# Kernel optimization log

Measured on AMD Instinct MI355X. Metric: run time of the kernel, lower is better.

## Reference

```python
import jax, jax.numpy as jnp
import numpy as np

B, N, DIM, HEADS = 1, 4096, 1024, 16
HEAD_DIM = DIM // HEADS
SCALE = HEAD_DIM ** -0.5
GRID = 64  # GRID*GRID == N, power-of-2 Hilbert grid


def _hilbert_d2xy(n, d):
    # standard Hilbert curve distance->(x,y), vectorized in numpy
    rx = np.zeros_like(d)
    ry = np.zeros_like(d)
    x = np.zeros_like(d)
    y = np.zeros_like(d)
    t = d.copy()
    s = 1
    while s < n:
        rx = (t // 2) & 1
        ry = (t ^ rx) & 1
        # rotate
        swap = ry == 0
        flip = swap & (rx == 1)
        x_f = np.where(flip, s - 1 - x, x)
        y_f = np.where(flip, s - 1 - y, y)
        x, y = np.where(swap, y_f, x_f), np.where(swap, x_f, y_f)
        x = x + s * rx
        y = y + s * ry
        t = t // 4
        s *= 2
    return x, y


def _hilbert_indices(n_tokens, grid):
    d = np.arange(n_tokens)
    hx, hy = _hilbert_d2xy(grid, d)
    # token at Hilbert distance d lives at row-major position hy*grid+hx
    return (hy * grid + hx).astype(np.int32)


def setup_inputs() -> dict:
    key = jax.random.key(0)
    k1, k2, k3 = jax.random.split(key, 3)
    x = jax.random.normal(k1, (B, N, DIM), dtype=jnp.float32)
    w_qkv = jax.random.normal(k2, (3 * DIM, DIM), dtype=jnp.float32) * (DIM ** -0.5)
    w_out = jax.random.normal(k3, (DIM, DIM), dtype=jnp.float32) * (DIM ** -0.5)
    indices = jnp.asarray(_hilbert_indices(N, GRID))
    return {"x": x, "w_qkv": w_qkv, "w_out": w_out, "indices": indices}


def reference(x, w_qkv, w_out, indices):
    b, n, c = x.shape
    # qkv projection: nn.Linear -> x @ W^T, reshape to [B,N,3,H,Dh]
    qkv = jnp.einsum("bnc,dc->bnd", x, w_qkv).reshape(b, n, 3, HEADS, HEAD_DIM)
    q, k, v = qkv[:, :, 0], qkv[:, :, 1], qkv[:, :, 2]  # each [B,N,H,Dh]
    # Hilbert gather along sequence
    q = q[:, indices]
    k = k[:, indices]
    v = v[:, indices]
    # full softmax attention per head
    scores = jnp.einsum("bnhd,bmhd->bhnm", q, k) * SCALE
    attn = jax.nn.softmax(scores, axis=-1)
    out = jnp.einsum("bhnm,bmhd->bnhd", attn, v)  # [B,N,H,Dh]
    # scatter back to original order
    inv = jnp.argsort(indices)
    out = out[:, inv].reshape(b, n, c)
    return jnp.einsum("bnc,dc->bnd", out, w_out)
```

## Files before the change

kernel.cpp:

```cpp
#include <hip/hip_runtime.h>
#include <stdint.h>

#define NTOK 4096
#define HD 64
#define DIMC 1024

typedef __attribute__((ext_vector_type(8))) short s16x8;
typedef __attribute__((ext_vector_type(4))) float f32x4;

#if __has_builtin(__builtin_amdgcn_exp2f)
#define EXP2(x) __builtin_amdgcn_exp2f(x)
#else
#define EXP2(x) exp2f(x)
#endif

__device__ inline unsigned short f2bf(float f) {
  union { float f; unsigned u; } v; v.f = f;
  unsigned r = v.u + 0x7FFFu + ((v.u >> 16) & 1u);
  return (unsigned short)(r >> 16);
}

__device__ inline unsigned cvt_pk_bf16(float lo, float hi) {
  unsigned r;
  asm("v_cvt_pk_bf16_f32 %0, %1, %2" : "=v"(r) : "v"(lo), "v"(hi));
  return r;
}

__device__ inline float bf2f(unsigned short u) {
  union { unsigned u; float f; } v; v.u = ((unsigned)u) << 16;
  return v.f;
}

__device__ inline void gld16(const void* g, void* s) {
  __builtin_amdgcn_global_load_lds((const __attribute__((address_space(1))) void*)g,
                                   (__attribute__((address_space(3))) void*)s, 16, 0, 0);
}

#define N4_X   1048576
#define N4_WQ  786432
#define N4_WO  262144
__global__ void cvt_all(const float4* __restrict__ x, const float4* __restrict__ wq,
                        const float4* __restrict__ wo, ushort4* __restrict__ xb,
                        ushort4* __restrict__ wqb, ushort4* __restrict__ wob) {
  int i = blockIdx.x * 256 + threadIdx.x;
  const float4* s; ushort4* d; int off;
  if (i < N4_X) { s = x; d = xb; off = i; }
  else if (i < N4_X + N4_WQ) { s = wq; d = wqb; off = i - N4_X; }
  else { s = wo; d = wob; off = i - (N4_X + N4_WQ); }
  float4 v = s[off];
  ushort4 o;
  o.x = f2bf(v.x); o.y = f2bf(v.y); o.z = f2bf(v.z); o.w = f2bf(v.w);
  d[off] = o;
}

#define QSCALE 0.18033688011112042f
__global__ __launch_bounds__(256) void gemm_qkv(
    const unsigned short* __restrict__ A,
    const unsigned short* __restrict__ B,
    unsigned short* __restrict__ qb,
    unsigned short* __restrict__ kb,
    unsigned short* __restrict__ vtb)
{
  __shared__ unsigned short As[128 * 32];
  __shared__ unsigned short Bs[128 * 32];
  const int t = threadIdx.x;
  const int l = t & 63;
  const int w = t >> 6;
  const int wr = w >> 1, wc = w & 1;
  const int bm = blockIdx.x, bn = blockIdx.y;
  const int K = 1024;

  f32x4 acc[4][4];
#pragma unroll
  for (int m = 0; m < 4; ++m)
#pragma unroll
    for (int n = 0; n < 4; ++n)
#pragma unroll
      for (int r = 0; r < 4; ++r) acc[m][n][r] = 0.f;

  for (int kt = 0; kt < K; kt += 32) {
    __syncthreads();
#pragma unroll
    for (int j = 0; j < 2; ++j) {
      const int o = j * 4096 + t * 16;
      const int row = o >> 6;
      const int cole = (o & 63) >> 1;
      gld16(A + (size_t)(bm * 128 + row) * K + kt + cole, (char*)As + o);
      gld16(B + (size_t)(bn * 128 + row) * K + kt + cole, (char*)Bs + o);
    }
    __syncthreads();
    s16x8 af[4], bfr[4];
    const int cb = (l >> 4) * 16;
#pragma unroll
    for (int m = 0; m < 4; ++m)
      af[m] = *(const s16x8*)((const char*)As + (wr * 64 + m * 16 + (l & 15)) * 64 + cb);
#pragma unroll
    for (int n = 0; n < 4; ++n)
      bfr[n] = *(const s16x8*)((const char*)Bs + (wc * 64 + n * 16 + (l & 15)) * 64 + cb);
#pragma unroll
    for (int m = 0; m < 4; ++m)
#pragma unroll
      for (int n = 0; n < 4; ++n)
        acc[m][n] = __builtin_amdgcn_mfma_f32_16x16x32_bf16(af[m], bfr[n], acc[m][n], 0, 0, 0);
  }

#pragma unroll
  for (int m = 0; m < 4; ++m) {
#pragma unroll
    for (int n = 0; n < 4; ++n) {
#pragma unroll
      for (int r = 0; r < 4; ++r) {
        const int gm = bm * 128 + wr * 64 + m * 16 + (l >> 4) * 4 + r;
        const int gn = bn * 128 + wc * 64 + n * 16 + (l & 15);
        const float val = acc[m][n][r];
        const int part = gn >> 10;
        const int h = (gn >> 6) & 15;
        const int dd = gn & 63;
        if (part == 0)      qb[((size_t)h * NTOK + gm) * HD + dd] = f2bf(val * QSCALE);
        else if (part == 1) kb[((size_t)h * NTOK + gm) * HD + dd] = f2bf(val);
        else                vtb[((size_t)h * HD + dd) * NTOK + gm] = f2bf(val);
      }
    }
  }
}

__global__ __launch_bounds__(128, 4) void fa_split(
    const unsigned short* __restrict__ Q,
    const unsigned short* __restrict__ Kin,
    const unsigned short* __restrict__ Vt,
    unsigned short* __restrict__ Opart,
    float* __restrict__ Lpart)
{
  __shared__ unsigned short Ks[2][32 * 64];
  __shared__ unsigned short Vs[2][64 * 32];

  const int t = threadIdx.x, l = t & 63, w = t >> 6;
  const int g = l >> 4, q = l & 15;
  const int wg = blockIdx.x;
  const int h = wg & 15;
  const int qt = (wg >> 4) & 63;
  const int half = wg >> 10;
  const int q0 = qt * 64 + w * 32;
  const int kbase0 = half * (NTOK / 2);
  const unsigned short* Qh = Q + (size_t)h * NTOK * HD;
  const unsigned short* Kh = Kin + (size_t)h * NTOK * HD;
  const unsigned short* Vh = Vt + (size_t)h * HD * NTOK;

  int offK[2], offV[2];
#pragma unroll
  for (int j = 0; j < 2; ++j) {
    const int o = j * 2048 + t * 16;
    const int rho = o >> 7;
    const int c = o & 127;
    const int n = ((rho & 12) << 1) | ((rho & 16) >> 2) | (rho & 3);
    offK[j] = n * 128 + (c ^ ((rho & 7) << 4));
    const int rv = o >> 6;
    const int cv = o & 63;
    offV[j] = rv * (NTOK * 2) + (cv ^ (((rv >> 1) & 3) << 4));
  }

  s16x8 qf[2][2];
#pragma unroll
  for (int rb = 0; rb < 2; ++rb)
#pragma unroll
    for (int tq = 0; tq < 2; ++tq)
      qf[rb][tq] = *(const s16x8*)(Qh + (size_t)(q0 + rb * 16 + q) * HD + tq * 32 + g * 8);

  s16x8 ones;
#pragma unroll
  for (int i = 0; i < 8; ++i) ones[i] = (short)0x3F80;

  f32x4 oacc[2][4], lacc[2];
#pragma unroll
  for (int rb = 0; rb < 2; ++rb) {
#pragma unroll
    for (int db = 0; db < 4; ++db)
#pragma unroll
      for (int r = 0; r < 4; ++r) oacc[rb][db][r] = 0.f;
#pragma unroll
    for (int r = 0; r < 4; ++r) lacc[rb][r] = 0.f;
  }

#pragma unroll
  for (int j = 0; j < 2; ++j) {
    const int o = j * 2048 + t * 16;
    gld16((const char*)Kh + (size_t)kbase0 * 128 + offK[j], (char*)Ks[0] + o);
    gld16((const char*)Vh + (size_t)kbase0 * 2 + offV[j], (char*)Vs[0] + o);
  }
  __syncthreads();

  int cur = 0;
  const int NIT = (NTOK / 2) / 32;
  for (int it = 0; it < NIT; ++it) {
    if (it + 1 < NIT) {
      const char* kp = (const char*)Kh + (size_t)(kbase0 + (it + 1) * 32) * 128;
      const char* vp = (const char*)Vh + (size_t)(kbase0 + (it + 1) * 32) * 2;
#pragma unroll
      for (int j = 0; j < 2; ++j) {
        const int o = j * 2048 + t * 16;
        gld16(kp + offK[j], (char*)Ks[cur ^ 1] + o);
        gld16(vp + offV[j], (char*)Vs[cur ^ 1] + o);
      }
    }

    const char* kb = (const char*)Ks[cur];
    const char* vb = (const char*)Vs[cur];

    f32x4 sc[2][2];
    __builtin_amdgcn_s_setprio(1);
#pragma unroll
    for (int kb2 = 0; kb2 < 2; ++kb2) {
      const int row = kb2 * 16 + q;
      const int swz = (row & 7) << 4;
      s16x8 kf0 = *(const s16x8*)(kb + row * 128 + ((g * 16) ^ swz));
      s16x8 kf1 = *(const s16x8*)(kb + row * 128 + ((64 + g * 16) ^ swz));
#pragma unroll
      for (int rb = 0; rb < 2; ++rb) {
        f32x4 z = {0.f, 0.f, 0.f, 0.f};
        z = __builtin_amdgcn_mfma_f32_16x16x32_bf16(kf0, qf[rb][0], z, 0, 0, 0);
        sc[rb][kb2] = __builtin_amdgcn_mfma_f32_16x16x32_bf16(kf1, qf[rb][1], z, 0, 0, 0);
      }
    }
    __builtin_amdgcn_s_setprio(0);

    union PU { unsigned u[4]; s16x8 v; } pu[2];
#pragma unroll
    for (int rb = 0; rb < 2; ++rb) {
      pu[rb].u[0] = cvt_pk_bf16(EXP2(sc[rb][0][0]), EXP2(sc[rb][0][1]));
      pu[rb].u[1] = cvt_pk_bf16(EXP2(sc[rb][0][2]), EXP2(sc[rb][0][3]));
      pu[rb].u[2] = cvt_pk_bf16(EXP2(sc[rb][1][0]), EXP2(sc[rb][1][1]));
      pu[rb].u[3] = cvt_pk_bf16(EXP2(sc[rb][1][2]), EXP2(sc[rb][1][3]));
    }

    __builtin_amdgcn_s_setprio(1);
    const int vswz = ((q >> 1) & 3) << 4;
#pragma unroll
    for (int db = 0; db < 4; ++db) {
      const int row = db * 16 + q;
      s16x8 vf = *(const s16x8*)(vb + row * 64 + ((g * 16) ^ vswz));
#pragma unroll
      for (int rb = 0; rb < 2; ++rb)
        oacc[rb][db] = __builtin_amdgcn_mfma_f32_16x16x32_bf16(vf, pu[rb].v, oacc[rb][db], 0, 0, 0);
    }
#pragma unroll
    for (int rb = 0; rb < 2; ++rb)
      lacc[rb] = __builtin_amdgcn_mfma_f32_16x16x32_bf16(ones, pu[rb].v, lacc[rb], 0, 0, 0);
    __builtin_amdgcn_s_setprio(0);

    __syncthreads();
    cur ^= 1;
  }

  const size_t pbase = ((size_t)(half * 16 + h) * NTOK);
#pragma unroll
  for (int rb = 0; rb < 2; ++rb) {
    const int nn = q0 + rb * 16 + q;
#pragma unroll
    for (int db = 0; db < 4; ++db) {
      uint2 pr;
      pr.x = cvt_pk_bf16(oacc[rb][db][0], oacc[rb][db][1]);
      pr.y = cvt_pk_bf16(oacc[rb][db][2], oacc[rb][db][3]);
      *(uint2*)(Opart + (pbase + nn) * HD + db * 16 + g * 4) = pr;
    }
    if (g == 0) Lpart[pbase + nn] = lacc[rb][0];
  }
}

__global__ __launch_bounds__(256) void gemm_out(
    const unsigned short* __restrict__ Opart,
    const float* __restrict__ Lpart,
    const unsigned short* __restrict__ Bw,
    float* __restrict__ outf)
{
  __shared__ unsigned short As[128 * 32];
  __shared__ unsigned short Bs[128 * 32];
  const int t = threadIdx.x;
  const int l = t & 63;
  const int w = t >> 6;
  const int wr = w >> 1, wc = w & 1;
  const int bm = blockIdx.x, bn = blockIdx.y;

  f32x4 acc[4][4];
#pragma unroll
  for (int m = 0; m < 4; ++m)
#pragma unroll
    for (int n = 0; n < 4; ++n)
#pragma unroll
      for (int r = 0; r < 4; ++r) acc[m][n][r] = 0.f;

  for (int kt = 0; kt < 1024; kt += 32) {
    __syncthreads();
#pragma unroll
    for (int j = 0; j < 2; ++j) {
      const int o = j * 4096 + t * 16;
      const int row = o >> 6;
      const int cole = (o & 63) >> 1;
      gld16(Bw + (size_t)(bn * 128 + row) * 1024 + kt + cole, (char*)Bs + o);
      const int kg = kt + cole;
      const int hh = kg >> 6, dd = kg & 63;
      const int mm = bm * 128 + row;
      const size_t base = ((size_t)hh * NTOK + mm) * HD + dd;
      s16x8 p0 = *(const s16x8*)(Opart + base);
      s16x8 p1 = *(const s16x8*)(Opart + base + (size_t)16 * NTOK * HD);
      const float inv = 1.f / (Lpart[(size_t)hh * NTOK + mm] +
                               Lpart[(size_t)16 * NTOK + (size_t)hh * NTOK + mm]);
      union PA { unsigned u[4]; s16x8 v; } pa;
#pragma unroll
      for (int e = 0; e < 4; ++e)
        pa.u[e] = cvt_pk_bf16((bf2f((unsigned short)p0[2 * e]) + bf2f((unsigned short)p1[2 * e])) * inv,
                              (bf2f((unsigned short)p0[2 * e + 1]) + bf2f((unsigned short)p1[2 * e + 1])) * inv);
      *(s16x8*)((char*)As + o) = pa.v;
    }
    __syncthreads();
    s16x8 af[4], bfr[4];
    const int cb = (l >> 4) * 16;
#pragma unroll
    for (int m = 0; m < 4; ++m)
      af[m] = *(const s16x8*)((const char*)As + (wr * 64 + m * 16 + (l & 15)) * 64 + cb);
#pragma unroll
    for (int n = 0; n < 4; ++n)
      bfr[n] = *(const s16x8*)((const char*)Bs + (wc * 64 + n * 16 + (l & 15)) * 64 + cb);
#pragma unroll
    for (int m = 0; m < 4; ++m)
#pragma unroll
      for (int n = 0; n < 4; ++n)
        acc[m][n] = __builtin_amdgcn_mfma_f32_16x16x32_bf16(af[m], bfr[n], acc[m][n], 0, 0, 0);
  }

#pragma unroll
  for (int m = 0; m < 4; ++m)
#pragma unroll
    for (int n = 0; n < 4; ++n)
#pragma unroll
      for (int r = 0; r < 4; ++r) {
        const int gm = bm * 128 + wr * 64 + m * 16 + (l >> 4) * 4 + r;
        const int gn = bn * 128 + wc * 64 + n * 16 + (l & 15);
        outf[(size_t)gm * 1024 + gn] = acc[m][n][r];
      }
}

extern "C" void kernel_launch(void* const* d_in, const int* in_sizes, int n_in,
                              void* d_out, int out_size, void* d_ws, size_t ws_size,
                              hipStream_t stream) {
  const float* x    = (const float*)d_in[0];
  const float* wqkv = (const float*)d_in[1];
  const float* wout = (const float*)d_in[2];
  float* out = (float*)d_out;
  char* ws = (char*)d_ws;

  unsigned short* Opart = (unsigned short*)(ws);
  unsigned short* xb    = (unsigned short*)(ws);
  unsigned short* wqkvb = (unsigned short*)(ws + 8388608);
  float*          Lp    = (float*)(ws + 16777216);
  unsigned short* Qb    = (unsigned short*)(ws + 17825792);
  unsigned short* Kb    = (unsigned short*)(ws + 26214400);
  unsigned short* Vtb   = (unsigned short*)(ws + 34603008);
  unsigned short* woutb = (unsigned short*)(ws + 42991616);

  cvt_all<<<8192, 256, 0, stream>>>((const float4*)x, (const float4*)wqkv, (const float4*)wout,
                                    (ushort4*)xb, (ushort4*)wqkvb, (ushort4*)woutb);

  gemm_qkv<<<dim3(32, 24), 256, 0, stream>>>(xb, wqkvb, Qb, Kb, Vtb);

  fa_split<<<2048, 128, 0, stream>>>(Qb, Kb, Vtb, Opart, Lp);

  gemm_out<<<dim3(32, 8), 256, 0, stream>>>(Opart, Lp, woutb, out);
}
```

Measured before the change: 170.3 us.

## Enlarge attention query tile, split keys four ways, add separate combine kernel

```diff
diff --git a/kernel.cpp b/kernel.cpp
--- a/kernel.cpp
+++ b/kernel.cpp
@@ -38,15 +38,12 @@
 
 #define N4_X   1048576
 #define N4_WQ  786432
-#define N4_WO  262144
 __global__ void cvt_all(const float4* __restrict__ x, const float4* __restrict__ wq,
-                        const float4* __restrict__ wo, ushort4* __restrict__ xb,
-                        ushort4* __restrict__ wqb, ushort4* __restrict__ wob) {
+                        ushort4* __restrict__ xb, ushort4* __restrict__ wqb) {
   int i = blockIdx.x * 256 + threadIdx.x;
   const float4* s; ushort4* d; int off;
   if (i < N4_X) { s = x; d = xb; off = i; }
-  else if (i < N4_X + N4_WQ) { s = wq; d = wqb; off = i - N4_X; }
-  else { s = wo; d = wob; off = i - (N4_X + N4_WQ); }
+  else { s = wq; d = wqb; off = i - N4_X; }
   float4 v = s[off];
   ushort4 o;
   o.x = f2bf(v.x); o.y = f2bf(v.y); o.z = f2bf(v.z); o.w = f2bf(v.w);
@@ -124,7 +121,8 @@
   }
 }
 
-__global__ __launch_bounds__(128, 4) void fa_split(
+template<int S>
+__global__ __launch_bounds__(128, 2) void fa_split(
     const unsigned short* __restrict__ Q,
     const unsigned short* __restrict__ Kin,
     const unsigned short* __restrict__ Vt,
@@ -138,10 +136,12 @@
   const int g = l >> 4, q = l & 15;
   const int wg = blockIdx.x;
   const int h = wg & 15;
-  const int qt = (wg >> 4) & 63;
-  const int half = wg >> 10;
-  const int q0 = qt * 64 + w * 32;
-  const int kbase0 = half * (NTOK / 2);
+  const int qt = (wg >> 4) & 31;
+  const int split = wg >> 9;
+  const int q0 = qt * 128 + w * 64;
+  constexpr int KEYS = NTOK / S;
+  constexpr int NIT = KEYS / 32;
+  const int kstart = split * KEYS;
   const unsigned short* Qh = Q + (size_t)h * NTOK * HD;
   const unsigned short* Kh = Kin + (size_t)h * NTOK * HD;
   const unsigned short* Vh = Vt + (size_t)h * HD * NTOK;
@@ -159,9 +159,9 @@
     offV[j] = rv * (NTOK * 2) + (cv ^ (((rv >> 1) & 3) << 4));
   }
 
-  s16x8 qf[2][2];
-#pragma unroll
-  for (int rb = 0; rb < 2; ++rb)
+  s16x8 qf[4][2];
+#pragma unroll
+  for (int rb = 0; rb < 4; ++rb)
 #pragma unroll
     for (int tq = 0; tq < 2; ++tq)
       qf[rb][tq] = *(const s16x8*)(Qh + (size_t)(q0 + rb * 16 + q) * HD + tq * 32 + g * 8);
@@ -170,9 +170,9 @@
 #pragma unroll
   for (int i = 0; i < 8; ++i) ones[i] = (short)0x3F80;
 
-  f32x4 oacc[2][4], lacc[2];
-#pragma unroll
-  for (int rb = 0; rb < 2; ++rb) {
+  f32x4 oacc[4][4], lacc[4];
+#pragma unroll
+  for (int rb = 0; rb < 4; ++rb) {
 #pragma unroll
     for (int db = 0; db < 4; ++db)
 #pragma unroll
@@ -184,17 +184,16 @@
 #pragma unroll
   for (int j = 0; j < 2; ++j) {
     const int o = j * 2048 + t * 16;
-    gld16((const char*)Kh + (size_t)kbase0 * 128 + offK[j], (char*)Ks[0] + o);
-    gld16((const char*)Vh + (size_t)kbase0 * 2 + offV[j], (char*)Vs[0] + o);
+    gld16((const char*)Kh + (size_t)kstart * 128 + offK[j], (char*)Ks[0] + o);
+    gld16((const char*)Vh + (size_t)kstart * 2 + offV[j], (char*)Vs[0] + o);
   }
   __syncthreads();
 
   int cur = 0;
-  const int NIT = (NTOK / 2) / 32;
   for (int it = 0; it < NIT; ++it) {
     if (it + 1 < NIT) {
-      const char* kp = (const char*)Kh + (size_t)(kbase0 + (it + 1) * 32) * 128;
-      const char* vp = (const char*)Vh + (size_t)(kbase0 + (it + 1) * 32) * 2;
+      const char* kp = (const char*)Kh + (size_t)(kstart + (it + 1) * 32) * 128;
+      const char* vp = (const char*)Vh + (size_t)(kstart + (it + 1) * 32) * 2;
 #pragma unroll
       for (int j = 0; j < 2; ++j) {
         const int o = j * 2048 + t * 16;
@@ -206,7 +205,7 @@
     const char* kb = (const char*)Ks[cur];
     const char* vb = (const char*)Vs[cur];
 
-    f32x4 sc[2][2];
+    f32x4 sc[4][2];
     __builtin_amdgcn_s_setprio(1);
 #pragma unroll
     for (int kb2 = 0; kb2 < 2; ++kb2) {
@@ -215,7 +214,7 @@
       s16x8 kf0 = *(const s16x8*)(kb + row * 128 + ((g * 16) ^ swz));
       s16x8 kf1 = *(const s16x8*)(kb + row * 128 + ((64 + g * 16) ^ swz));
 #pragma unroll
-      for (int rb = 0; rb < 2; ++rb) {
+      for (int rb = 0; rb < 4; ++rb) {
         f32x4 z = {0.f, 0.f, 0.f, 0.f};
         z = __builtin_amdgcn_mfma_f32_16x16x32_bf16(kf0, qf[rb][0], z, 0, 0, 0);
         sc[rb][kb2] = __builtin_amdgcn_mfma_f32_16x16x32_bf16(kf1, qf[rb][1], z, 0, 0, 0);
@@ -223,9 +222,9 @@
     }
     __builtin_amdgcn_s_setprio(0);
 
-    union PU { unsigned u[4]; s16x8 v; } pu[2];
-#pragma unroll
-    for (int rb = 0; rb < 2; ++rb) {
+    union PU { unsigned u[4]; s16x8 v; } pu[4];
+#pragma unroll
+    for (int rb = 0; rb < 4; ++rb) {
       pu[rb].u[0] = cvt_pk_bf16(EXP2(sc[rb][0][0]), EXP2(sc[rb][0][1]));
       pu[rb].u[1] = cvt_pk_bf16(EXP2(sc[rb][0][2]), EXP2(sc[rb][0][3]));
       pu[rb].u[2] = cvt_pk_bf16(EXP2(sc[rb][1][0]), EXP2(sc[rb][1][1]));
@@ -239,11 +238,11 @@
       const int row = db * 16 + q;
       s16x8 vf = *(const s16x8*)(vb + row * 64 + ((g * 16) ^ vswz));
 #pragma unroll
-      for (int rb = 0; rb < 2; ++rb)
+      for (int rb = 0; rb < 4; ++rb)
         oacc[rb][db] = __builtin_amdgcn_mfma_f32_16x16x32_bf16(vf, pu[rb].v, oacc[rb][db], 0, 0, 0);
     }
 #pragma unroll
-    for (int rb = 0; rb < 2; ++rb)
+    for (int rb = 0; rb < 4; ++rb)
       lacc[rb] = __builtin_amdgcn_mfma_f32_16x16x32_bf16(ones, pu[rb].v, lacc[rb], 0, 0, 0);
     __builtin_amdgcn_s_setprio(0);
 
@@ -251,9 +250,9 @@
     cur ^= 1;
   }
 
-  const size_t pbase = ((size_t)(half * 16 + h) * NTOK);
-#pragma unroll
-  for (int rb = 0; rb < 2; ++rb) {
+  const size_t pbase = ((size_t)(split * 16 + h) * NTOK);
+#pragma unroll
+  for (int rb = 0; rb < 4; ++rb) {
     const int nn = q0 + rb * 16 + q;
 #pragma unroll
     for (int db = 0; db < 4; ++db) {
@@ -266,10 +265,37 @@
   }
 }
 
-__global__ __launch_bounds__(256) void gemm_out(
+template<int S>
+__global__ __launch_bounds__(256) void fa_combine(
     const unsigned short* __restrict__ Opart,
     const float* __restrict__ Lpart,
-    const unsigned short* __restrict__ Bw,
+    unsigned short* __restrict__ O)
+{
+  const int tid = blockIdx.x * 256 + threadIdx.x;
+  const int d4 = tid & 15;
+  const int n = (tid >> 4) & 4095;
+  const int h = tid >> 16;
+  const size_t stride = (size_t)16 * NTOK * HD;
+  const size_t e0 = ((size_t)h * NTOK + n) * HD + d4 * 4;
+  float a0 = 0.f, a1 = 0.f, a2 = 0.f, a3 = 0.f, ls = 0.f;
+#pragma unroll
+  for (int s = 0; s < S; ++s) {
+    ushort4 p = *(const ushort4*)(Opart + e0 + s * stride);
+    a0 += bf2f(p.x); a1 += bf2f(p.y); a2 += bf2f(p.z); a3 += bf2f(p.w);
+    ls += Lpart[(size_t)s * 16 * NTOK + (size_t)h * NTOK + n];
+  }
+  const float inv = 1.f / ls;
+  ushort4 o;
+  o.x = f2bf(a0 * inv);
+  o.y = f2bf(a1 * inv);
+  o.z = f2bf(a2 * inv);
+  o.w = f2bf(a3 * inv);
+  *(ushort4*)(O + (size_t)n * DIMC + h * HD + d4 * 4) = o;
+}
+
+__global__ __launch_bounds__(256) void gemm_out(
+    const unsigned short* __restrict__ A,
+    const float* __restrict__ wout,
     float* __restrict__ outf)
 {
   __shared__ unsigned short As[128 * 32];
@@ -295,21 +321,16 @@
       const int o = j * 4096 + t * 16;
       const int row = o >> 6;
       const int cole = (o & 63) >> 1;
-      gld16(Bw + (size_t)(bn * 128 + row) * 1024 + kt + cole, (char*)Bs + o);
-      const int kg = kt + cole;
-      const int hh = kg >> 6, dd = kg & 63;
-      const int mm = bm * 128 + row;
-      const size_t base = ((size_t)hh * NTOK + mm) * HD + dd;
-      s16x8 p0 = *(const s16x8*)(Opart + base);
-      s16x8 p1 = *(const s16x8*)(Opart + base + (size_t)16 * NTOK * HD);
-      const float inv = 1.f / (Lpart[(size_t)hh * NTOK + mm] +
-                               Lpart[(size_t)16 * NTOK + (size_t)hh * NTOK + mm]);
-      union PA { unsigned u[4]; s16x8 v; } pa;
-#pragma unroll
-      for (int e = 0; e < 4; ++e)
-        pa.u[e] = cvt_pk_bf16((bf2f((unsigned short)p0[2 * e]) + bf2f((unsigned short)p1[2 * e])) * inv,
-                              (bf2f((unsigned short)p0[2 * e + 1]) + bf2f((unsigned short)p1[2 * e + 1])) * inv);
-      *(s16x8*)((char*)As + o) = pa.v;
+      gld16(A + (size_t)(bm * 128 + row) * 1024 + kt + cole, (char*)As + o);
+      const float* bsrc = wout + (size_t)(bn * 128 + row) * 1024 + kt + cole;
+      float4 b0 = *(const float4*)bsrc;
+      float4 b1 = *(const float4*)(bsrc + 4);
+      union PB { unsigned u[4]; s16x8 v; } pb;
+      pb.u[0] = cvt_pk_bf16(b0.x, b0.y);
+      pb.u[1] = cvt_pk_bf16(b0.z, b0.w);
+      pb.u[2] = cvt_pk_bf16(b1.x, b1.y);
+      pb.u[3] = cvt_pk_bf16(b1.z, b1.w);
+      *(s16x8*)((char*)Bs + o) = pb.v;
     }
     __syncthreads();
     s16x8 af[4], bfr[4];
@@ -348,21 +369,39 @@
   float* out = (float*)d_out;
   char* ws = (char*)d_ws;
 
-  unsigned short* Opart = (unsigned short*)(ws);
-  unsigned short* xb    = (unsigned short*)(ws);
-  unsigned short* wqkvb = (unsigned short*)(ws + 8388608);
-  float*          Lp    = (float*)(ws + 16777216);
-  unsigned short* Qb    = (unsigned short*)(ws + 17825792);
-  unsigned short* Kb    = (unsigned short*)(ws + 26214400);
-  unsigned short* Vtb   = (unsigned short*)(ws + 34603008);
-  unsigned short* woutb = (unsigned short*)(ws + 42991616);
-
-  cvt_all<<<8192, 256, 0, stream>>>((const float4*)x, (const float4*)wqkv, (const float4*)wout,
-                                    (ushort4*)xb, (ushort4*)wqkvb, (ushort4*)woutb);
-
-  gemm_qkv<<<dim3(32, 24), 256, 0, stream>>>(xb, wqkvb, Qb, Kb, Vtb);
-
-  fa_split<<<2048, 128, 0, stream>>>(Qb, Kb, Vtb, Opart, Lp);
-
-  gemm_out<<<dim3(32, 8), 256, 0, stream>>>(Opart, Lp, woutb, out);
-}
+  const bool big = ws_size >= 59768832ull;
+
+  if (big) {
+    unsigned short* Opart = (unsigned short*)(ws);
+    unsigned short* xb    = (unsigned short*)(ws);
+    unsigned short* wqkvb = (unsigned short*)(ws + 8388608);
+    float*          Lp    = (float*)(ws + 33554432);
+    unsigned short* Qb    = (unsigned short*)(ws + 34603008);
+    unsigned short* Kb    = (unsigned short*)(ws + 42991616);
+    unsigned short* Vtb   = (unsigned short*)(ws + 51380224);
+    unsigned short* aob   = Qb;
+
+    cvt_all<<<7168, 256, 0, stream>>>((const float4*)x, (const float4*)wqkv,
+                                      (ushort4*)xb, (ushort4*)wqkvb);
+    gemm_qkv<<<dim3(32, 24), 256, 0, stream>>>(xb, wqkvb, Qb, Kb, Vtb);
+    fa_split<4><<<2048, 128, 0, stream>>>(Qb, Kb, Vtb, Opart, Lp);
+    fa_combine<4><<<4096, 256, 0, stream>>>(Opart, Lp, aob);
+    gemm_out<<<dim3(32, 8), 256, 0, stream>>>(aob, wout, out);
+  } else {
+    unsigned short* Opart = (unsigned short*)(ws);
+    unsigned short* xb    = (unsigned short*)(ws);
+    unsigned short* wqkvb = (unsigned short*)(ws + 8388608);
+    float*          Lp    = (float*)(ws + 16777216);
+    unsigned short* Qb    = (unsigned short*)(ws + 17825792);
+    unsigned short* Kb    = (unsigned short*)(ws + 26214400);
+    unsigned short* Vtb   = (unsigned short*)(ws + 34603008);
+    unsigned short* aob   = Qb;
+
+    cvt_all<<<7168, 256, 0, stream>>>((const float4*)x, (const float4*)wqkv,
+                                      (ushort4*)xb, (ushort4*)wqkvb);
+    gemm_qkv<<<dim3(32, 24), 256, 0, stream>>>(xb, wqkvb, Qb, Kb, Vtb);
+    fa_split<2><<<1024, 128, 0, stream>>>(Qb, Kb, Vtb, Opart, Lp);
+    fa_combine<2><<<4096, 256, 0, stream>>>(Opart, Lp, aob);
+    gemm_out<<<dim3(32, 8), 256, 0, stream>>>(aob, wout, out);
+  }
+}
```

Measured after the change: 168.8 us. Within noise of the previous version (-0.9%).

## Use explicit vmcnt waits in flash loop and split combine from output GEMM

Applied to the files above, without the earlier changes.

```diff
diff --git a/kernel.cpp b/kernel.cpp
--- a/kernel.cpp
+++ b/kernel.cpp
@@ -38,15 +38,12 @@
 
 #define N4_X   1048576
 #define N4_WQ  786432
-#define N4_WO  262144
 __global__ void cvt_all(const float4* __restrict__ x, const float4* __restrict__ wq,
-                        const float4* __restrict__ wo, ushort4* __restrict__ xb,
-                        ushort4* __restrict__ wqb, ushort4* __restrict__ wob) {
+                        ushort4* __restrict__ xb, ushort4* __restrict__ wqb) {
   int i = blockIdx.x * 256 + threadIdx.x;
   const float4* s; ushort4* d; int off;
   if (i < N4_X) { s = x; d = xb; off = i; }
-  else if (i < N4_X + N4_WQ) { s = wq; d = wqb; off = i - N4_X; }
-  else { s = wo; d = wob; off = i - (N4_X + N4_WQ); }
+  else { s = wq; d = wqb; off = i - N4_X; }
   float4 v = s[off];
   ushort4 o;
   o.x = f2bf(v.x); o.y = f2bf(v.y); o.z = f2bf(v.z); o.w = f2bf(v.w);
@@ -201,7 +198,13 @@
         gld16(kp + offK[j], (char*)Ks[cur ^ 1] + o);
         gld16(vp + offV[j], (char*)Vs[cur ^ 1] + o);
       }
-    }
+      asm volatile("s_waitcnt vmcnt(4)" ::: "memory");
+    } else {
+      asm volatile("s_waitcnt vmcnt(0)" ::: "memory");
+    }
+    __builtin_amdgcn_sched_barrier(0);
+    __builtin_amdgcn_s_barrier();
+    __builtin_amdgcn_sched_barrier(0);
 
     const char* kb = (const char*)Ks[cur];
     const char* vb = (const char*)Vs[cur];
@@ -247,7 +250,9 @@
       lacc[rb] = __builtin_amdgcn_mfma_f32_16x16x32_bf16(ones, pu[rb].v, lacc[rb], 0, 0, 0);
     __builtin_amdgcn_s_setprio(0);
 
-    __syncthreads();
+    __builtin_amdgcn_sched_barrier(0);
+    __builtin_amdgcn_s_barrier();
+    __builtin_amdgcn_sched_barrier(0);
     cur ^= 1;
   }
 
@@ -266,10 +271,31 @@
   }
 }
 
-__global__ __launch_bounds__(256) void gemm_out(
+__global__ __launch_bounds__(256) void fa_combine(
     const unsigned short* __restrict__ Opart,
     const float* __restrict__ Lpart,
-    const unsigned short* __restrict__ Bw,
+    unsigned short* __restrict__ O)
+{
+  const int tid = blockIdx.x * 256 + threadIdx.x;
+  const int d4 = tid & 15;
+  const int n = (tid >> 4) & 4095;
+  const int h = tid >> 16;
+  const size_t stride = (size_t)16 * NTOK * HD;
+  const size_t e0 = ((size_t)h * NTOK + n) * HD + d4 * 4;
+  ushort4 a = *(const ushort4*)(Opart + e0);
+  ushort4 b = *(const ushort4*)(Opart + e0 + stride);
+  const float inv = 1.f / (Lpart[(size_t)h * NTOK + n] + Lpart[(size_t)16 * NTOK + (size_t)h * NTOK + n]);
+  ushort4 o;
+  o.x = f2bf((bf2f(a.x) + bf2f(b.x)) * inv);
+  o.y = f2bf((bf2f(a.y) + bf2f(b.y)) * inv);
+  o.z = f2bf((bf2f(a.z) + bf2f(b.z)) * inv);
+  o.w = f2bf((bf2f(a.w) + bf2f(b.w)) * inv);
+  *(ushort4*)(O + (size_t)n * DIMC + h * HD + d4 * 4) = o;
+}
+
+__global__ __launch_bounds__(256) void gemm_out(
+    const unsigned short* __restrict__ A,
+    const float* __restrict__ wout,
     float* __restrict__ outf)
 {
   __shared__ unsigned short As[128 * 32];
@@ -295,21 +321,16 @@
       const int o = j * 4096 + t * 16;
       const int row = o >> 6;
       const int cole = (o & 63) >> 1;
-      gld16(Bw + (size_t)(bn * 128 + row) * 1024 + kt + cole, (char*)Bs + o);
-      const int kg = kt + cole;
-      const int hh = kg >> 6, dd = kg & 63;
-      const int mm = bm * 128 + row;
-      const size_t base = ((size_t)hh * NTOK + mm) * HD + dd;
-      s16x8 p0 = *(const s16x8*)(Opart + base);
-      s16x8 p1 = *(const s16x8*)(Opart + base + (size_t)16 * NTOK * HD);
-      const float inv = 1.f / (Lpart[(size_t)hh * NTOK + mm] +
-                               Lpart[(size_t)16 * NTOK + (size_t)hh * NTOK + mm]);
-      union PA { unsigned u[4]; s16x8 v; } pa;
-#pragma unroll
-      for (int e = 0; e < 4; ++e)
-        pa.u[e] = cvt_pk_bf16((bf2f((unsigned short)p0[2 * e]) + bf2f((unsigned short)p1[2 * e])) * inv,
-                              (bf2f((unsigned short)p0[2 * e + 1]) + bf2f((unsigned short)p1[2 * e + 1])) * inv);
-      *(s16x8*)((char*)As + o) = pa.v;
+      gld16(A + (size_t)(bm * 128 + row) * 1024 + kt + cole, (char*)As + o);
+      const float* bsrc = wout + (size_t)(bn * 128 + row) * 1024 + kt + cole;
+      float4 b0 = *(const float4*)bsrc;
+      float4 b1 = *(const float4*)(bsrc + 4);
+      union PB { unsigned u[4]; s16x8 v; } pb;
+      pb.u[0] = cvt_pk_bf16(b0.x, b0.y);
+      pb.u[1] = cvt_pk_bf16(b0.z, b0.w);
+      pb.u[2] = cvt_pk_bf16(b1.x, b1.y);
+      pb.u[3] = cvt_pk_bf16(b1.z, b1.w);
+      *(s16x8*)((char*)Bs + o) = pb.v;
     }
     __syncthreads();
     s16x8 af[4], bfr[4];
@@ -355,14 +376,16 @@
   unsigned short* Qb    = (unsigned short*)(ws + 17825792);
   unsigned short* Kb    = (unsigned short*)(ws + 26214400);
   unsigned short* Vtb   = (unsigned short*)(ws + 34603008);
-  unsigned short* woutb = (unsigned short*)(ws + 42991616);
-
-  cvt_all<<<8192, 256, 0, stream>>>((const float4*)x, (const float4*)wqkv, (const float4*)wout,
-                                    (ushort4*)xb, (ushort4*)wqkvb, (ushort4*)woutb);
+  unsigned short* aob   = Qb;
+
+  cvt_all<<<7168, 256, 0, stream>>>((const float4*)x, (const float4*)wqkv,
+                                    (ushort4*)xb, (ushort4*)wqkvb);
 
   gemm_qkv<<<dim3(32, 24), 256, 0, stream>>>(xb, wqkvb, Qb, Kb, Vtb);
 
   fa_split<<<2048, 128, 0, stream>>>(Qb, Kb, Vtb, Opart, Lp);
 
-  gemm_out<<<dim3(32, 8), 256, 0, stream>>>(Opart, Lp, woutb, out);
-}
+  fa_combine<<<4096, 256, 0, stream>>>(Opart, Lp, aob);
+
+  gemm_out<<<dim3(32, 8), 256, 0, stream>>>(aob, wout, out);
+}
```

New measurement: 166.8 us. 1.02x faster.
